# Kernel tuning notes

Measured on AMD Instinct MI355X. Metric: run time of the kernel, lower is better.

Reference implementation:

```python
import jax, jax.numpy as jnp
import numpy as np

NUM_NODES = 8192
MUL = 64
ENV_P = 6
EPSILON = 1.0 / np.sqrt(17.0)  # 1/sqrt(1 + avg_num_neighbors), avg_num_neighbors=16


def _envelope(u, p=ENV_P):
    # polynomial smoothing envelope (cutoff at u = 1)
    a = -(p + 1) * (p + 2) / 2.0
    b = p * (p + 2)
    c = -p * (p + 1) / 2.0
    f = 1.0 + a * u ** p + b * u ** (p + 1) + c * u ** (p + 2)
    return jnp.where(u < 1.0, f, 0.0)


def setup_inputs() -> dict:
    key = jax.random.key(0)
    ks = jax.random.split(key, 9)
    E, F = 131072, 512
    vectors = jax.random.normal(ks[0], (E, 3), jnp.float32) * 0.35  # mostly inside cutoff
    x = jax.random.normal(ks[1], (E, F), jnp.float32)
    V = jax.random.normal(ks[2], (E, MUL, 4), jnp.float32)  # per mul-channel: [0e | 1o(3)]
    senders = jax.random.randint(ks[3], (E,), 0, NUM_NODES, jnp.int32)
    W_w = jax.random.normal(ks[4], (F, MUL), jnp.float32)
    W1 = jax.random.normal(ks[5], (F + 2 * MUL, 512), jnp.float32)
    W2 = jax.random.normal(ks[6], (512, 512), jnp.float32)
    W3 = jax.random.normal(ks[7], (512, 512), jnp.float32)
    W_lin = jax.random.normal(ks[8], (3 * MUL, MUL), jnp.float32)
    return {"vectors": vectors, "x": x, "V": V, "senders": senders,
            "W_w": W_w, "W1": W1, "W2": W2, "W3": W3, "W_lin": W_lin}


def reference(vectors, x, V, senders, W_w, W1, W2, W3, W_lin):
    E = vectors.shape[0]
    # edge-wise linear producing tensor-product weights  [E, MUL]
    w = (x @ W_w) / np.sqrt(x.shape[-1])
    # spherical harmonics (component norm), l = 0..1 of normalized vectors -> [E, 4]
    r = jnp.linalg.norm(vectors, axis=-1, keepdims=True)          # [E, 1]
    nhat = vectors / r
    Y = jnp.concatenate([jnp.ones((E, 1), vectors.dtype), np.sqrt(3.0) * nhat], axis=1)
    # weighted SH, scatter-sum over senders, gather back (map_back=True), scale by epsilon
    wY_e = w[:, :, None] * Y[:, None, :]                          # [E, MUL, 4]
    agg = jax.ops.segment_sum(wY_e, senders, num_segments=NUM_NODES)
    wY = agg[senders] * EPSILON                                   # [E, MUL, 4]
    # CG tensor product wY (0e+1o) x V (0e+1o), keep 0e and 1o outputs
    a0, a1 = wY[..., 0], wY[..., 1:]
    b0, b1 = V[..., 0], V[..., 1:]
    scal = jnp.concatenate(
        [a0 * b0, jnp.einsum('emi,emi->em', a1, b1) / np.sqrt(3.0)], axis=-1)  # [E, 2*MUL]
    vecs = jnp.concatenate(
        [a0[..., None] * b1, a1 * b0[..., None], jnp.cross(a1, b1) / np.sqrt(2.0)],
        axis=1)                                                   # [E, 3*MUL, 3]
    # concat scalar channel into invariants, 3-layer MLP (silu, linear last)
    xc = jnp.concatenate([x, scal], axis=1)                       # [E, 640]
    h = jax.nn.silu(xc @ W1 / np.sqrt(xc.shape[-1]))
    h = jax.nn.silu(h @ W2 / np.sqrt(h.shape[-1]))
    h = h @ W3 / np.sqrt(h.shape[-1])
    x_out = _envelope(r) * h                                      # [E, 512]
    # equivariant linear over the 1o multiplicity axis
    V_out = jnp.einsum('ekc,km->emc', vecs, W_lin) / np.sqrt(vecs.shape[1])  # [E, MUL, 3]
    return x_out, V_out
```

## Files before the change

### kernel.cpp

```cpp
#include <hip/hip_runtime.h>
#include <cstdint>
#include <cstddef>

#define E_TOT 131072
#define NNODES 8192

typedef __attribute__((ext_vector_type(8))) short bf16x8;
typedef __attribute__((ext_vector_type(4))) float f32x4;
typedef unsigned short u16;
typedef unsigned int u32;

__device__ __forceinline__ u16 f2bf(float f) {
    u32 u = __builtin_bit_cast(u32, f);
    u32 r = (u + 0x7FFFu + ((u >> 16) & 1u)) >> 16;
    return (u16)r;
}

__device__ __forceinline__ void gload16(const u16* g, u16* l) {
    __builtin_amdgcn_global_load_lds((const __attribute__((address_space(1))) void*)g,
                                     (__attribute__((address_space(3))) void*)l, 16, 0, 0);
}

__device__ __forceinline__ bf16x8 lds_frag(const u16* base, int row, int bytecol) {
    return *(const bf16x8*)((const char*)base + row * 128 + (bytecol ^ ((row & 7) << 4)));
}

__global__ void wconv_kernel(const float* __restrict__ src, u16* __restrict__ dst,
                             int K, int N) {
    int idx = blockIdx.x * 256 + threadIdx.x;
    if (idx >= N * K) return;
    int n = idx / K, k = idx - n * K;
    dst[idx] = f2bf(src[(size_t)k * N + n]);
}

__global__ void envy_kernel(const float* __restrict__ vectors, float* __restrict__ env,
                            float4* __restrict__ Y) {
    int e = blockIdx.x * 256 + threadIdx.x;
    float vx = vectors[3 * e + 0], vy = vectors[3 * e + 1], vz = vectors[3 * e + 2];
    float r2 = vx * vx + vy * vy + vz * vz;
    float r = sqrtf(r2);
    float u6 = r2 * r2 * r2;
    float f = 1.0f + u6 * (-28.0f + 48.0f * r - 21.0f * r2);
    env[e] = (r < 1.0f) ? f : 0.0f;
    float inv = 1.7320508075688772f / r;
    Y[e] = make_float4(1.0f, vx * inv, vy * inv, vz * inv);
}

__global__ void hist_kernel(const int* __restrict__ senders, int* __restrict__ cnt) {
    int e = blockIdx.x * 256 + threadIdx.x;
    atomicAdd(&cnt[senders[e]], 1);
}

__launch_bounds__(1024)
__global__ void scan_kernel(const int* __restrict__ cnt, int* __restrict__ off,
                            int* __restrict__ curs) {
    __shared__ int part[1024];
    const int t = threadIdx.x;
    int local[8];
    int s = 0;
#pragma unroll
    for (int j = 0; j < 8; ++j) { local[j] = cnt[t * 8 + j]; s += local[j]; }
    part[t] = s;
    __syncthreads();
    for (int d = 1; d < 1024; d <<= 1) {
        int v = (t >= d) ? part[t - d] : 0;
        __syncthreads();
        part[t] += v;
        __syncthreads();
    }
    int run = part[t] - s;
#pragma unroll
    for (int j = 0; j < 8; ++j) {
        off[t * 8 + j] = run;
        curs[t * 8 + j] = run;
        run += local[j];
    }
    if (t == 1023) off[8192] = run;
}

__global__ void permbuild_kernel(const int* __restrict__ senders, int* __restrict__ curs,
                                 int* __restrict__ perm) {
    int e = blockIdx.x * 256 + threadIdx.x;
    int s = senders[e];
    int p = atomicAdd(&curs[s], 1);
    perm[p] = e;
}

__launch_bounds__(256)
__global__ void gather_kernel(const float* __restrict__ w, const float4* __restrict__ Y,
                              const int* __restrict__ off, const int* __restrict__ perm,
                              float4* __restrict__ agg) {
    const int t = threadIdx.x;
    const int n = blockIdx.x * 4 + (t >> 6);
    const int m = t & 63;
    const int beg = off[n], end = off[n + 1];
    float4 acc = make_float4(0.f, 0.f, 0.f, 0.f);
    for (int i = beg; i < end; ++i) {
        int e = perm[i];
        float wv = w[(size_t)e * 64 + m];
        float4 y = Y[e];
        acc.x += wv * y.x; acc.y += wv * y.y; acc.z += wv * y.z; acc.w += wv * y.w;
    }
    agg[(size_t)n * 64 + m] = acc;
}

__launch_bounds__(256)
__global__ void wgemm_kernel(const float* __restrict__ x, const u16* __restrict__ Wt,
                             u16* __restrict__ XB, float* __restrict__ w) {
    __shared__ u16 As[128 * 72];
    __shared__ u16 Bs[64 * 72];
    const int e0 = blockIdx.x * 128;
    const int t = threadIdx.x, lane = t & 63, wid = t >> 6;
    const int lr = lane & 15, lh = lane >> 4;
    const int r8 = t >> 3, c8 = t & 7;
    f32x4 acc[2][4] = {};
    for (int kt = 0; kt < 8; ++kt) {
        const int kk = kt << 6;
#pragma unroll
        for (int i = 0; i < 4; ++i) {
            int row = i * 32 + r8;
            const float* gx = x + (size_t)(e0 + row) * 512 + kk + c8 * 8;
            float4 a = *(const float4*)gx;
            float4 b = *(const float4*)(gx + 4);
            union { u16 h[8]; uint4 v; } p;
            p.h[0] = f2bf(a.x); p.h[1] = f2bf(a.y); p.h[2] = f2bf(a.z); p.h[3] = f2bf(a.w);
            p.h[4] = f2bf(b.x); p.h[5] = f2bf(b.y); p.h[6] = f2bf(b.z); p.h[7] = f2bf(b.w);
            *(uint4*)((char*)As + row * 144 + c8 * 16) = p.v;
            *(uint4*)(XB + (size_t)(e0 + row) * 512 + kk + c8 * 8) = p.v;
        }
#pragma unroll
        for (int i = 0; i < 2; ++i) {
            int row = i * 32 + r8;
            const u16* g = Wt + (size_t)row * 512 + kk + c8 * 8;
            *(uint4*)((char*)Bs + row * 144 + c8 * 16) = *(const uint4*)g;
        }
        __syncthreads();
#pragma unroll
        for (int k2 = 0; k2 < 2; ++k2) {
            bf16x8 af[2], bfr[4];
#pragma unroll
            for (int m = 0; m < 2; ++m)
                af[m] = *(const bf16x8*)((const char*)As + (wid * 32 + m * 16 + lr) * 144 + k2 * 64 + lh * 16);
#pragma unroll
            for (int n = 0; n < 4; ++n)
                bfr[n] = *(const bf16x8*)((const char*)Bs + (n * 16 + lr) * 144 + k2 * 64 + lh * 16);
#pragma unroll
            for (int m = 0; m < 2; ++m)
#pragma unroll
                for (int n = 0; n < 4; ++n)
                    acc[m][n] = __builtin_amdgcn_mfma_f32_16x16x32_bf16(af[m], bfr[n], acc[m][n], 0, 0, 0);
        }
        __syncthreads();
    }
    const float s = 0.044194173824159216f;
#pragma unroll
    for (int m = 0; m < 2; ++m)
#pragma unroll
        for (int n = 0; n < 4; ++n)
#pragma unroll
            for (int j = 0; j < 4; ++j) {
                int e = e0 + wid * 32 + m * 16 + lh * 4 + j;
                w[(size_t)e * 64 + n * 16 + lr] = acc[m][n][j] * s;
            }
}

__launch_bounds__(256)
__global__ void edge_kernel(const int* __restrict__ senders, const float4* __restrict__ agg4,
                            const float4* __restrict__ V4, const u16* __restrict__ Wlt,
                            u16* __restrict__ scal, float* __restrict__ Vout) {
    __shared__ u16 a_lds[3][32][200];
    __shared__ u16 w_lds[64 * 200];
    const int t = threadIdx.x;
    const int e0 = blockIdx.x * 32;
#pragma unroll
    for (int i = 0; i < 6; ++i) {
        int c = i * 256 + t;
        int row = c / 24, off = (c % 24) * 8;
        *(uint4*)((char*)w_lds + row * 400 + off * 2) = ((const uint4*)Wlt)[c];
    }
    const float invs3 = 0.5773502691896258f;
    const float invs2 = 0.7071067811865476f;
    const float EPS = 0.24253562503633297f;
#pragma unroll
    for (int i = 0; i < 8; ++i) {
        int el = i * 4 + (t >> 6);
        int m = t & 63;
        int e = e0 + el;
        int s = senders[e];
        float4 a = agg4[(size_t)s * 64 + m];
        a.x *= EPS; a.y *= EPS; a.z *= EPS; a.w *= EPS;
        float4 b = V4[(size_t)e * 64 + m];
        float s0 = a.x * b.x;
        float s1 = (a.y * b.y + a.z * b.z + a.w * b.w) * invs3;
        scal[(size_t)e * 128 + m] = f2bf(s0);
        scal[(size_t)e * 128 + 64 + m] = f2bf(s1);
        float cx = (a.z * b.w - a.w * b.z) * invs2;
        float cy = (a.w * b.y - a.y * b.w) * invs2;
        float cz = (a.y * b.z - a.z * b.y) * invs2;
        a_lds[0][el][m] = f2bf(a.x * b.y);
        a_lds[0][el][64 + m] = f2bf(a.y * b.x);
        a_lds[0][el][128 + m] = f2bf(cx);
        a_lds[1][el][m] = f2bf(a.x * b.z);
        a_lds[1][el][64 + m] = f2bf(a.z * b.x);
        a_lds[1][el][128 + m] = f2bf(cy);
        a_lds[2][el][m] = f2bf(a.x * b.w);
        a_lds[2][el][64 + m] = f2bf(a.w * b.x);
        a_lds[2][el][128 + m] = f2bf(cz);
    }
    __syncthreads();
    const int lane = t & 63, wid = t >> 6;
    const int lr = lane & 15, lh = lane >> 4;
    f32x4 acc[3][2] = {};
    for (int kt = 0; kt < 6; ++kt) {
        bf16x8 bfr = *(const bf16x8*)((const char*)w_lds + (wid * 16 + lr) * 400 + kt * 64 + lh * 16);
#pragma unroll
        for (int c = 0; c < 3; ++c)
#pragma unroll
            for (int m = 0; m < 2; ++m) {
                bf16x8 afr = *(const bf16x8*)((const char*)a_lds + ((c * 32 + m * 16 + lr) * 400) + kt * 64 + lh * 16);
                acc[c][m] = __builtin_amdgcn_mfma_f32_16x16x32_bf16(afr, bfr, acc[c][m], 0, 0, 0);
            }
    }
    __syncthreads();
    float* ot = (float*)a_lds;
    const float sc = 0.07216878364870323f;
#pragma unroll
    for (int c = 0; c < 3; ++c)
#pragma unroll
        for (int m = 0; m < 2; ++m)
#pragma unroll
            for (int j = 0; j < 4; ++j) {
                int row = m * 16 + lh * 4 + j;
                int mul = wid * 16 + lr;
                ot[row * 192 + mul * 3 + c] = acc[c][m][j] * sc;
            }
    __syncthreads();
    float4* vo = (float4*)(Vout + (size_t)e0 * 192);
#pragma unroll
    for (int i = 0; i < 6; ++i)
        vo[i * 256 + t] = ((float4*)ot)[i * 256 + t];
}

template <int MODE, int K>
__launch_bounds__(256, 2)
__global__ void mlp_gemm(const u16* __restrict__ A, const u16* __restrict__ A2,
                         const u16* __restrict__ Bt, const float scale,
                         const float* __restrict__ env,
                         u16* __restrict__ outb, float* __restrict__ outf) {
    constexpr int NKT = K >> 6;
    __shared__ u16 lds[2][2][128 * 64];
    const int nwg = gridDim.x;
    const int bid = blockIdx.x;
    const int swz = (bid & 7) * (nwg >> 3) + (bid >> 3);
    const int mt = swz >> 2, nt = swz & 3;
    const int e0 = mt << 7, n0 = nt << 7;
    const int t = threadIdx.x, lane = t & 63, wid = t >> 6;
    const int wm = wid >> 1, wn = wid & 1;
    const int lr = lane & 15, lh = lane >> 4;
    f32x4 acc[4][4] = {};

    auto issue = [&](int kt) {
        const int kk = kt << 6;
        const int buf = kt & 1;
#pragma unroll
        for (int i = 0; i < 4; ++i) {
            const int c = i * 256 + t;
            const int rowin = c >> 3;
            const int scol = ((c & 7) ^ (rowin & 7)) << 3;
            const u16* gp;
            if (A2 && kk >= 512) gp = A2 + (size_t)(e0 + rowin) * 128 + (kk - 512) + scol;
            else                 gp = A + (size_t)(e0 + rowin) * 512 + kk + scol;
            gload16(gp, (u16*)&lds[buf][0][0] + (size_t)c * 8);
        }
#pragma unroll
        for (int i = 0; i < 4; ++i) {
            const int c = i * 256 + t;
            const int rowin = c >> 3;
            const int scol = ((c & 7) ^ (rowin & 7)) << 3;
            gload16(Bt + (size_t)(n0 + rowin) * K + kk + scol,
                    (u16*)&lds[buf][1][0] + (size_t)c * 8);
        }
    };

    issue(0);
    issue(1);
    for (int kt = 0; kt < NKT; ++kt) {
        if (kt + 1 < NKT) asm volatile("s_waitcnt vmcnt(8)\ns_barrier" ::: "memory");
        else              asm volatile("s_waitcnt vmcnt(0)\ns_barrier" ::: "memory");
        const u16* Ab = lds[kt & 1][0];
        const u16* Bb = lds[kt & 1][1];
        __builtin_amdgcn_s_setprio(1);
#pragma unroll
        for (int k2 = 0; k2 < 2; ++k2) {
            bf16x8 af[4], bfr[4];
#pragma unroll
            for (int m = 0; m < 4; ++m)
                af[m] = lds_frag(Ab, wm * 64 + m * 16 + lr, k2 * 64 + lh * 16);
#pragma unroll
            for (int n = 0; n < 4; ++n)
                bfr[n] = lds_frag(Bb, wn * 64 + n * 16 + lr, k2 * 64 + lh * 16);
#pragma unroll
            for (int m = 0; m < 4; ++m)
#pragma unroll
                for (int n = 0; n < 4; ++n)
                    acc[m][n] = __builtin_amdgcn_mfma_f32_16x16x32_bf16(af[m], bfr[n], acc[m][n], 0, 0, 0);
        }
        __builtin_amdgcn_s_setprio(0);
        if (kt + 2 < NKT) {
            asm volatile("s_waitcnt lgkmcnt(0)\ns_barrier" ::: "memory");
            issue(kt + 2);
        }
    }

#pragma unroll
    for (int m = 0; m < 4; ++m) {
#pragma unroll
        for (int j = 0; j < 4; ++j) {
            const int row = e0 + wm * 64 + m * 16 + lh * 4 + j;
            float ev = (MODE == 1) ? env[row] : 0.0f;
#pragma unroll
            for (int n = 0; n < 4; ++n) {
                const int col = n0 + wn * 64 + n * 16 + lr;
                float v = acc[m][n][j] * scale;
                if (MODE == 0) {
                    float sv = v / (1.0f + __expf(-v));
                    outb[(size_t)row * 512 + col] = f2bf(sv);
                } else {
                    outf[(size_t)row * 512 + col] = v * ev;
                }
            }
        }
    }
}

extern "C" void kernel_launch(void* const* d_in, const int* in_sizes, int n_in,
                              void* d_out, int out_size, void* d_ws, size_t ws_size,
                              hipStream_t stream) {
    const float* vectors = (const float*)d_in[0];
    const float* x       = (const float*)d_in[1];
    const float* V       = (const float*)d_in[2];
    const int*   senders = (const int*)d_in[3];
    const float* W_w     = (const float*)d_in[4];
    const float* W1      = (const float*)d_in[5];
    const float* W2      = (const float*)d_in[6];
    const float* W3      = (const float*)d_in[7];
    const float* W_lin   = (const float*)d_in[8];
    float* out = (float*)d_out;
    char* ws = (char*)d_ws;

    u16*    XB   = (u16*)(ws + 0x0);
    u16*    H1   = (u16*)(ws + 0x8000000);
    u16*    SCAL = (u16*)(ws + 0x10000000);
    float*  AGG  = (float*)(ws + 0x12000000);
    float*  ENV  = (float*)(ws + 0x12800000);
    float4* Yb   = (float4*)(ws + 0x12880000);
    float*  Wbuf = (float*)(ws + 0x12A80000);
    u16*    WT   = (u16*)(ws + 0x14A80000);
    u16* Wwt = WT;
    u16* W1t = Wwt + 64 * 512;
    u16* W2t = W1t + 512 * 640;
    u16* W3t = W2t + 512 * 512;
    u16* Wlt = W3t + 512 * 512;
    u16* H2 = XB;
    int* COUNT = (int*)(ws + 0x15000000);
    int* OFF   = (int*)(ws + 0x15010000);
    int* CURS  = (int*)(ws + 0x15020000);
    int* PERM  = (int*)(ws + 0x15030000);

    hipMemsetAsync(COUNT, 0, NNODES * sizeof(int), stream);

    wconv_kernel<<<(64 * 512) / 256, 256, 0, stream>>>(W_w, Wwt, 512, 64);
    wconv_kernel<<<(512 * 640) / 256, 256, 0, stream>>>(W1, W1t, 640, 512);
    wconv_kernel<<<(512 * 512) / 256, 256, 0, stream>>>(W2, W2t, 512, 512);
    wconv_kernel<<<(512 * 512) / 256, 256, 0, stream>>>(W3, W3t, 512, 512);
    wconv_kernel<<<(64 * 192) / 256, 256, 0, stream>>>(W_lin, Wlt, 192, 64);

    envy_kernel<<<E_TOT / 256, 256, 0, stream>>>(vectors, ENV, Yb);

    hist_kernel<<<E_TOT / 256, 256, 0, stream>>>(senders, COUNT);
    scan_kernel<<<1, 1024, 0, stream>>>(COUNT, OFF, CURS);
    permbuild_kernel<<<E_TOT / 256, 256, 0, stream>>>(senders, CURS, PERM);

    wgemm_kernel<<<E_TOT / 128, 256, 0, stream>>>(x, Wwt, XB, Wbuf);
    gather_kernel<<<NNODES / 4, 256, 0, stream>>>(Wbuf, Yb, OFF, PERM, (float4*)AGG);

    edge_kernel<<<E_TOT / 32, 256, 0, stream>>>(senders, (const float4*)AGG, (const float4*)V,
                                                Wlt, SCAL, out + (size_t)E_TOT * 512);

    const float s640 = 0.03952847075210474f;
    const float s512 = 0.044194173824159216f;
    const int gemm_grid = (E_TOT / 128) * 4;
    mlp_gemm<0, 640><<<gemm_grid, 256, 0, stream>>>(XB, SCAL, W1t, s640, nullptr, H1, nullptr);
    mlp_gemm<0, 512><<<gemm_grid, 256, 0, stream>>>(H1, nullptr, W2t, s512, nullptr, H2, nullptr);
    mlp_gemm<1, 512><<<gemm_grid, 256, 0, stream>>>(H2, nullptr, W3t, s512, ENV, nullptr, out);
}
```

Measured before the change: 617.8 us.

## Replace LDS-staged MLP GEMM with per-wave direct-to-register 64x64 tiles

Rewrites the MLP GEMM so each wave independently computes a 64x64 output tile, loading A and B fragments straight from global memory into registers with a two-stage software pipeline. This removes LDS staging, the swizzled global_load_lds transfers and the block-level barriers, and raises the occupancy hint to 3 blocks per CU. In exchange, operands are no longer shared across the four waves of a block, so global and L2 traffic per FLOP roughly doubles and the loads are less coalesced.

```diff
diff --git a/kernel.cpp b/kernel.cpp
--- a/kernel.cpp
+++ b/kernel.cpp
@@ -14,15 +14,6 @@
     u32 u = __builtin_bit_cast(u32, f);
     u32 r = (u + 0x7FFFu + ((u >> 16) & 1u)) >> 16;
     return (u16)r;
-}
-
-__device__ __forceinline__ void gload16(const u16* g, u16* l) {
-    __builtin_amdgcn_global_load_lds((const __attribute__((address_space(1))) void*)g,
-                                     (__attribute__((address_space(3))) void*)l, 16, 0, 0);
-}
-
-__device__ __forceinline__ bf16x8 lds_frag(const u16* base, int row, int bytecol) {
-    return *(const bf16x8*)((const char*)base + row * 128 + (bytecol ^ ((row & 7) << 4)));
 }
 
 __global__ void wconv_kernel(const float* __restrict__ src, u16* __restrict__ dst,
@@ -242,86 +233,65 @@
 }
 
 template <int MODE, int K>
-__launch_bounds__(256, 2)
+__launch_bounds__(256, 3)
 __global__ void mlp_gemm(const u16* __restrict__ A, const u16* __restrict__ A2,
                          const u16* __restrict__ Bt, const float scale,
                          const float* __restrict__ env,
                          u16* __restrict__ outb, float* __restrict__ outf) {
-    constexpr int NKT = K >> 6;
-    __shared__ u16 lds[2][2][128 * 64];
+    constexpr int NKT = K >> 5;
     const int nwg = gridDim.x;
     const int bid = blockIdx.x;
     const int swz = (bid & 7) * (nwg >> 3) + (bid >> 3);
-    const int mt = swz >> 2, nt = swz & 3;
-    const int e0 = mt << 7, n0 = nt << 7;
     const int t = threadIdx.x, lane = t & 63, wid = t >> 6;
-    const int wm = wid >> 1, wn = wid & 1;
+    const int gw = swz * 4 + wid;
+    const int ntile = gw & 7, mtile = gw >> 3;
+    const int e0 = mtile << 6, n0 = ntile << 6;
     const int lr = lane & 15, lh = lane >> 4;
     f32x4 acc[4][4] = {};
 
-    auto issue = [&](int kt) {
-        const int kk = kt << 6;
-        const int buf = kt & 1;
-#pragma unroll
-        for (int i = 0; i < 4; ++i) {
-            const int c = i * 256 + t;
-            const int rowin = c >> 3;
-            const int scol = ((c & 7) ^ (rowin & 7)) << 3;
-            const u16* gp;
-            if (A2 && kk >= 512) gp = A2 + (size_t)(e0 + rowin) * 128 + (kk - 512) + scol;
-            else                 gp = A + (size_t)(e0 + rowin) * 512 + kk + scol;
-            gload16(gp, (u16*)&lds[buf][0][0] + (size_t)c * 8);
-        }
-#pragma unroll
-        for (int i = 0; i < 4; ++i) {
-            const int c = i * 256 + t;
-            const int rowin = c >> 3;
-            const int scol = ((c & 7) ^ (rowin & 7)) << 3;
-            gload16(Bt + (size_t)(n0 + rowin) * K + kk + scol,
-                    (u16*)&lds[buf][1][0] + (size_t)c * 8);
+    bf16x8 a0[4], b0[4], a1[4], b1[4];
+
+    auto loadA = [&](bf16x8* d, int kk) {
+#pragma unroll
+        for (int fi = 0; fi < 4; ++fi) {
+            const u16* p;
+            if (A2 && kk >= 512) p = A2 + (size_t)(e0 + fi * 16 + lr) * 128 + (kk - 512) + lh * 8;
+            else                 p = A + (size_t)(e0 + fi * 16 + lr) * 512 + kk + lh * 8;
+            d[fi] = *(const bf16x8*)p;
         }
     };
-
-    issue(0);
-    issue(1);
-    for (int kt = 0; kt < NKT; ++kt) {
-        if (kt + 1 < NKT) asm volatile("s_waitcnt vmcnt(8)\ns_barrier" ::: "memory");
-        else              asm volatile("s_waitcnt vmcnt(0)\ns_barrier" ::: "memory");
-        const u16* Ab = lds[kt & 1][0];
-        const u16* Bb = lds[kt & 1][1];
-        __builtin_amdgcn_s_setprio(1);
-#pragma unroll
-        for (int k2 = 0; k2 < 2; ++k2) {
-            bf16x8 af[4], bfr[4];
-#pragma unroll
-            for (int m = 0; m < 4; ++m)
-                af[m] = lds_frag(Ab, wm * 64 + m * 16 + lr, k2 * 64 + lh * 16);
-#pragma unroll
-            for (int n = 0; n < 4; ++n)
-                bfr[n] = lds_frag(Bb, wn * 64 + n * 16 + lr, k2 * 64 + lh * 16);
-#pragma unroll
-            for (int m = 0; m < 4; ++m)
-#pragma unroll
-                for (int n = 0; n < 4; ++n)
-                    acc[m][n] = __builtin_amdgcn_mfma_f32_16x16x32_bf16(af[m], bfr[n], acc[m][n], 0, 0, 0);
-        }
-        __builtin_amdgcn_s_setprio(0);
-        if (kt + 2 < NKT) {
-            asm volatile("s_waitcnt lgkmcnt(0)\ns_barrier" ::: "memory");
-            issue(kt + 2);
-        }
-    }
-
-#pragma unroll
-    for (int m = 0; m < 4; ++m) {
+    auto loadB = [&](bf16x8* d, int kk) {
+#pragma unroll
+        for (int nf = 0; nf < 4; ++nf)
+            d[nf] = *(const bf16x8*)(Bt + (size_t)(n0 + nf * 16 + lr) * K + kk + lh * 8);
+    };
+    auto mfma16 = [&](const bf16x8* af, const bf16x8* bfr) {
+#pragma unroll
+        for (int fi = 0; fi < 4; ++fi)
+#pragma unroll
+            for (int nf = 0; nf < 4; ++nf)
+                acc[fi][nf] = __builtin_amdgcn_mfma_f32_16x16x32_bf16(af[fi], bfr[nf], acc[fi][nf], 0, 0, 0);
+    };
+
+    loadA(a0, 0); loadB(b0, 0);
+#pragma unroll 1
+    for (int kt = 0; kt < NKT; kt += 2) {
+        if (kt + 1 < NKT) { loadA(a1, (kt + 1) << 5); loadB(b1, (kt + 1) << 5); }
+        mfma16(a0, b0);
+        if (kt + 2 < NKT) { loadA(a0, (kt + 2) << 5); loadB(b0, (kt + 2) << 5); }
+        if (kt + 1 < NKT) mfma16(a1, b1);
+    }
+
+#pragma unroll
+    for (int fi = 0; fi < 4; ++fi) {
 #pragma unroll
         for (int j = 0; j < 4; ++j) {
-            const int row = e0 + wm * 64 + m * 16 + lh * 4 + j;
+            const int row = e0 + fi * 16 + lh * 4 + j;
             float ev = (MODE == 1) ? env[row] : 0.0f;
 #pragma unroll
-            for (int n = 0; n < 4; ++n) {
-                const int col = n0 + wn * 64 + n * 16 + lr;
-                float v = acc[m][n][j] * scale;
+            for (int nf = 0; nf < 4; ++nf) {
+                const int col = n0 + nf * 16 + lr;
+                float v = acc[fi][nf][j] * scale;
                 if (MODE == 0) {
                     float sv = v / (1.0f + __expf(-v));
                     outb[(size_t)row * 512 + col] = f2bf(sv);
@@ -389,7 +359,7 @@
 
     const float s640 = 0.03952847075210474f;
     const float s512 = 0.044194173824159216f;
-    const int gemm_grid = (E_TOT / 128) * 4;
+    const int gemm_grid = (E_TOT / 64) * 8 / 4;
     mlp_gemm<0, 640><<<gemm_grid, 256, 0, stream>>>(XB, SCAL, W1t, s640, nullptr, H1, nullptr);
     mlp_gemm<0, 512><<<gemm_grid, 256, 0, stream>>>(H1, nullptr, W2t, s512, nullptr, H2, nullptr);
     mlp_gemm<1, 512><<<gemm_grid, 256, 0, stream>>>(H2, nullptr, W3t, s512, ENV, nullptr, out);
```

After: 1.043 ms. 1.69x slower.
